# Performance work log

Measured on AMD Instinct MI355X. Metric: run time of the kernel, lower is better.

The kernel has to match this reference:

```python
import jax, jax.numpy as jnp
import numpy as np

B, N, F = 64, 512, 30          # batch, pf candidates, raw features
NDIM0, NDIM = 2, 4             # coord dims: layer0 uses 2, rest use n_dim_gnn=4
NOUT, NLAYERS = 64, 5          # GNN layer width / count
NDENSE = 128
BN_EPS = 1e-3                  # keras BatchNormalization default epsilon


def setup_inputs() -> dict:
    key = jax.random.key(0)
    ks = jax.random.split(key, 20)
    xx = jax.random.normal(ks[0], (B, N, F), jnp.float32)
    # validity mask: first L_b candidates valid
    lengths = jax.random.randint(ks[1], (B,), N // 4, N + 1)
    valid = (jnp.arange(N)[None, :] < lengths[:, None]).astype(jnp.float32)
    pt = jax.random.randint(ks[2], (B, N), 0, 8).astype(jnp.float32)
    pvq = jax.random.randint(ks[3], (B, N), 0, 8).astype(jnp.float32)
    fpv = jax.random.randint(ks[4], (B, N), 0, 4).astype(jnp.float32)
    xx = xx.at[:, :, 0].set(valid).at[:, :, 27].set(pt).at[:, :, 28].set(pvq).at[:, :, 29].set(fpv)
    g = lambda k, s, sc=0.05: jax.random.normal(k, s, jnp.float32) * sc
    d_in0 = 33  # 2+2+2 embeddings + 27 float features
    return {
        "xx": xx,
        "emb1": g(ks[5], (8, 2), 0.5),
        "emb2": g(ks[6], (8, 2), 0.5),
        "emb3": g(ks[7], (4, 2), 0.5),
        "A0": g(ks[8], ((d_in0 + 1) * 2 - 1, NOUT)),   # [67,64]
        "b0": g(ks[9], (NOUT,)),
        "A_rest": g(ks[10], (NLAYERS - 1, (NOUT + 1) * 2 - 1, NOUT)),  # [4,129,64]
        "b_rest": g(ks[11], (NLAYERS - 1, NOUT)),
        "bn_gamma": jnp.ones((NLAYERS, NOUT), jnp.float32),
        "bn_beta": jnp.zeros((NLAYERS, NOUT), jnp.float32),
        "dW0": g(ks[12], (N * NOUT, NDENSE), 0.01),
        "db0": g(ks[13], (NDENSE,)),
        "dW1": g(ks[14], (NDENSE, NDENSE)),
        "db1": g(ks[15], (NDENSE,)),
        "dbn_gamma": jnp.ones((2, NDENSE), jnp.float32),
        "dbn_beta": jnp.zeros((2, NDENSE), jnp.float32),
        "W2": g(ks[16], (NDENSE, 2)),
        "b2": g(ks[17], (2,)),
    }


def _bn(x, g, b):
    # inference BatchNorm with moving_mean=0, moving_var=1 (initial stats)
    return g * x * (1.0 / jnp.sqrt(1.0 + BN_EPS)) + b


def _gnn_layer(x, mask, n_dim, A, b):
    # x: [B,N,Fin], mask: [B,N]. Original builds [B,N,N,Fin+1] via tile/reshape;
    # algebraically the reduction over senders i factorizes:
    #   ss_feat[b,j] = x[b,j] * mask[b,j] * sum_i exp(-10*d_ij)
    #   ss_last[b,j] = mask[b,j] * sum_i d_ij * exp(-10*d_ij)
    c = x[..., -n_dim:]
    diff = c[:, :, None, :] - c[:, None, :, :]      # [B,N,N,n_dim]
    dist = jnp.sum(diff * diff, axis=-1)            # [B,N,N] squared distance
    w = jnp.exp(-10.0 * dist)
    S = jnp.sum(w, axis=1)                          # [B,N] per receiver j
    T = jnp.sum(dist * w, axis=1)                   # [B,N]
    ss_feat = x * (mask * S)[..., None] - x         # subtract concat(x, 0)
    ss_last = (mask * T)[..., None]
    xcat = jnp.concatenate([x, ss_feat, ss_last], axis=-1)  # [B,N,2*Fin+1]
    return (xcat @ A + b) * mask[..., None]


def _forward(xx, emb1, emb2, emb3, A0, b0, A_rest, b_rest, bn_gamma, bn_beta,
             dW0, db0, dW1, db1, dbn_gamma, dbn_beta, W2, b2):
    mask = xx[:, :, 0]
    e1 = emb1[jnp.abs(xx[:, :, 27]).astype(jnp.int32)]
    e2 = emb2[jnp.abs(xx[:, :, 28]).astype(jnp.int32)]
    e3 = emb3[jnp.abs(xx[:, :, 29]).astype(jnp.int32)]
    x = jnp.concatenate([e1, e2, e3, xx[:, :, :27]], axis=-1)  # [B,N,33]
    x = jnp.tanh(_bn(_gnn_layer(x, mask, NDIM0, A0, b0), bn_gamma[0], bn_beta[0]))
    for k in range(NLAYERS - 1):
        x = _gnn_layer(x, mask, NDIM, A_rest[k], b_rest[k])
        x = jnp.tanh(_bn(x, bn_gamma[k + 1], bn_beta[k + 1]))
    x = x.reshape(B, N * NOUT)
    x = jax.nn.sigmoid(_bn(x @ dW0 + db0, dbn_gamma[0], dbn_beta[0]))
    x = jax.nn.sigmoid(_bn(x @ dW1 + db1, dbn_gamma[1], dbn_beta[1]))
    x = x @ W2 + b2                                  # [B,2]
    # mode == 'dm': concat zeros on the right
    return jnp.concatenate([x, jnp.zeros((B, 2), x.dtype)], axis=1)


def reference(xx, emb1, emb2, emb3, A0, b0, A_rest, b_rest, bn_gamma, bn_beta,
              dW0, db0, dW1, db1, dbn_gamma, dbn_beta, W2, b2):
    return _forward(xx, emb1, emb2, emb3, A0, b0, A_rest, b_rest, bn_gamma, bn_beta,
                    dW0, db0, dW1, db1, dbn_gamma, dbn_beta, W2, b2)
```

## Files before the change

kernel.cpp:

```cpp
#include <hip/hip_runtime.h>
#include <math.h>

#define B_ 64
#define N_ 512
#define R_ (B_*N_)
#define INV_S 0.9995003746877732f

__device__ __forceinline__ float fast_tanh(float y){
  return 1.f - 2.f*__builtin_amdgcn_rcpf(1.f + __expf(2.f*y));
}
__device__ __forceinline__ float fast_sigmoid(float v){
  return __builtin_amdgcn_rcpf(1.f + __expf(-v));
}

struct GnnArgs {
  const float* xx;
  const float* emb1; const float* emb2; const float* emb3;
  const float* A0;  const float* b0;
  const float* Ar;  const float* br;
  const float* bng; const float* bnb;
  float4* cb0; float4* cb1;
  unsigned int* bar;
  float* xfinal;
};

template<int KP>
__device__ __forceinline__ void gemm_tile(const float* __restrict__ alo,
                                          const float* __restrict__ ahi,
                                          const float* __restrict__ xsrc,
                                          int o0, int lr0,
                                          float4 acc1[2], float4 acc2[2])
{
#pragma unroll
  for (int rr=0;rr<2;rr++){
    acc1[rr] = make_float4(0.f,0.f,0.f,0.f);
    acc2[rr] = make_float4(0.f,0.f,0.f,0.f);
  }
#pragma unroll 2
  for (int kc = 0; kc < KP; kc += 4){
    float4 a1[4], a2[4], xv[2];
#pragma unroll
    for (int uu=0;uu<4;uu++){
      a1[uu] = *(const float4*)&alo[(kc+uu)*64 + o0];
      a2[uu] = *(const float4*)&ahi[(kc+uu)*64 + o0];
    }
#pragma unroll
    for (int rr=0;rr<2;rr++)
      xv[rr] = *(const float4*)&xsrc[(lr0+rr)*68 + kc];
#pragma unroll
    for (int uu=0;uu<4;uu++){
#pragma unroll
      for (int rr=0;rr<2;rr++){
        float xu = ((const float*)&xv[rr])[uu];
        acc1[rr].x = fmaf(xu, a1[uu].x, acc1[rr].x);
        acc1[rr].y = fmaf(xu, a1[uu].y, acc1[rr].y);
        acc1[rr].z = fmaf(xu, a1[uu].z, acc1[rr].z);
        acc1[rr].w = fmaf(xu, a1[uu].w, acc1[rr].w);
        acc2[rr].x = fmaf(xu, a2[uu].x, acc2[rr].x);
        acc2[rr].y = fmaf(xu, a2[uu].y, acc2[rr].y);
        acc2[rr].z = fmaf(xu, a2[uu].z, acc2[rr].z);
        acc2[rr].w = fmaf(xu, a2[uu].w, acc2[rr].w);
      }
    }
  }
}

__global__ __launch_bounds__(512, 4) void gnn_fused(GnnArgs g)
{
  __shared__ float alo[64*64];
  __shared__ float ahi[64*64];
  __shared__ float xs[64*68];
  __shared__ float4 cl[512];
  __shared__ float spart[512], tpart[512];
  __shared__ float ml[64];

  const int tid   = threadIdx.x;
  const int b     = blockIdx.x;
  const int jc    = blockIdx.y;
  const int jloc  = jc*64;
  const int rbase = b*N_;
  const int cg = tid & 15, rg = tid >> 4;
  const int o0 = cg*4,  lr0 = rg*2;
  unsigned int* barp = g.bar + b*32;

  for (int k = 0; k < 5; ++k){
    const float* A;  const float* bi;  int K;
    if (k == 0){ A = g.A0;                        bi = g.b0;            K = 33; }
    else       { A = g.Ar + (size_t)(k-1)*129*64; bi = g.br + (k-1)*64; K = 64; }
    const float* gam = g.bng + k*64;
    const float* bet = g.bnb + k*64;

    if (k == 0){
      for (int idx = tid; idx < 36*64; idx += 512){
        int f = idx >> 6;
        alo[idx] = (f < 33) ? A[idx] : 0.f;
        ahi[idx] = (f < 33) ? A[33*64 + idx] : 0.f;
      }
      {
        const float* xr = g.xx + (size_t)(rbase + tid)*30;
        cl[tid] = make_float4(xr[25], xr[26], 0.f, 0.f);
      }
      if (tid < 64){
        const float* row = g.xx + (size_t)(rbase + jloc + tid)*30;
        float v[30];
#pragma unroll
        for (int i=0;i<30;i++) v[i] = row[i];
        int i1 = (int)fabsf(v[27]);
        int i2 = (int)fabsf(v[28]);
        int i3 = (int)fabsf(v[29]);
        float* o = &xs[tid*68];
        o[0]=g.emb1[i1*2+0]; o[1]=g.emb1[i1*2+1];
        o[2]=g.emb2[i2*2+0]; o[3]=g.emb2[i2*2+1];
        o[4]=g.emb3[i3*2+0]; o[5]=g.emb3[i3*2+1];
#pragma unroll
        for (int i=0;i<27;i++) o[6+i] = v[i];
        o[33]=0.f; o[34]=0.f; o[35]=0.f;
        ml[tid] = v[0];
      }
    } else {
      __syncthreads();
      if (tid == 0){
        __builtin_amdgcn_fence(__ATOMIC_RELEASE, "agent");
        __hip_atomic_fetch_add(barp, 1u, __ATOMIC_RELAXED, __HIP_MEMORY_SCOPE_AGENT);
      }
      {
        const float4* A4 = (const float4*)A;
        float4* alo4 = (float4*)alo;
        float4* ahi4 = (float4*)ahi;
        for (int idx = tid; idx < 1024; idx += 512){
          alo4[idx] = A4[idx];
          ahi4[idx] = A4[1024 + idx];
        }
      }
    }
    __syncthreads();

    float4 acc1[2], acc2[2];
    if (k == 0) gemm_tile<36>(alo, ahi, xs, o0, lr0, acc1, acc2);
    else        gemm_tile<64>(alo, ahi, xs, o0, lr0, acc1, acc2);

    float4 alast = *(const float4*)&A[(size_t)2*K*64 + o0];
    float4 bo = *(const float4*)&bi[o0];
    float4 go = *(const float4*)&gam[o0];
    float4 bb = *(const float4*)&bet[o0];

    if (k >= 1){
      if (tid == 0){
        unsigned int tgt = 8u*(unsigned int)k;
        while (__hip_atomic_load(barp, __ATOMIC_RELAXED, __HIP_MEMORY_SCOPE_AGENT) < tgt)
          __builtin_amdgcn_s_sleep(2);
        __builtin_amdgcn_fence(__ATOMIC_ACQUIRE, "agent");
      }
      __syncthreads();
      const float4* cbr = ((k & 1) ? g.cb0 : g.cb1) + rbase;
      cl[tid] = cbr[tid];
      __syncthreads();
    }

    {
      int jj = tid & 63, ic = tid >> 6, base = ic*64;
      float Ss = 0.f, Ts = 0.f;
      if (k == 0){
        float4 cj = cl[jloc + jj];
#pragma unroll 8
        for (int i=0;i<64;i++){
          float4 ci = cl[base+i];
          float d0 = cj.x-ci.x, d1 = cj.y-ci.y;
          float dist = d0*d0 + d1*d1;
          float w = __expf(-10.f*dist);
          Ss += w; Ts += dist*w;
        }
      } else {
        float4 cj = cl[jloc + jj];
#pragma unroll 8
        for (int i=0;i<64;i++){
          float4 ci = cl[base+i];
          float d0 = cj.x-ci.x, d1 = cj.y-ci.y, d2 = cj.z-ci.z, d3 = cj.w-ci.w;
          float dist = d0*d0 + d1*d1 + d2*d2 + d3*d3;
          float w = __expf(-10.f*dist);
          Ss += w; Ts += dist*w;
        }
      }
      spart[tid] = Ss;
      tpart[tid] = Ts;
    }
    __syncthreads();

    float4* cbw = (k & 1) ? g.cb1 : g.cb0;
#pragma unroll
    for (int rr=0;rr<2;rr++){
      int lr = lr0 + rr;
      float S = 0.f, T = 0.f;
#pragma unroll
      for (int c=0;c<8;c++){
        S += spart[lr + 64*c];
        T += tpart[lr + 64*c];
      }
      float m = ml[lr];
      float sc = m*S - 1.f;
      float tc = m*T;
      float4 v;
      v.x = (acc1[rr].x + sc*acc2[rr].x + tc*alast.x + bo.x)*m;
      v.y = (acc1[rr].y + sc*acc2[rr].y + tc*alast.y + bo.y)*m;
      v.z = (acc1[rr].z + sc*acc2[rr].z + tc*alast.z + bo.z)*m;
      v.w = (acc1[rr].w + sc*acc2[rr].w + tc*alast.w + bo.w)*m;
      float4 t;
      t.x = fast_tanh(go.x*(v.x*INV_S) + bb.x);
      t.y = fast_tanh(go.y*(v.y*INV_S) + bb.y);
      t.z = fast_tanh(go.z*(v.z*INV_S) + bb.z);
      t.w = fast_tanh(go.w*(v.w*INV_S) + bb.w);
      if (k < 4){
        *(float4*)&xs[lr*68 + o0] = t;
        if (cg == 15) cbw[rbase + jloc + lr] = t;
      } else {
        *(float4*)&g.xfinal[(size_t)(rbase + jloc + lr)*64 + o0] = t;
      }
    }
  }
}

__global__ __launch_bounds__(256) void dense0_partial(
    const float* __restrict__ X, const float* __restrict__ W,
    float* __restrict__ partial)
{
  __shared__ float xt[64*32];
  __shared__ float wt[32*128];
  int tid = threadIdx.x;
  int k0 = blockIdx.x*128;
  int og = (tid & 15)*8;
  int rg = (tid >> 4)*4;
  float acc[4][8];
#pragma unroll
  for (int a=0;a<4;a++)
#pragma unroll
    for (int u=0;u<8;u++) acc[a][u]=0.f;
  for (int kt = 0; kt < 128; kt += 32){
    __syncthreads();
    for (int idx = tid; idx < 512; idx += 256){
      int r = idx >> 3, kq = idx & 7;
      *(float4*)&xt[r*32 + kq*4] =
          *(const float4*)&X[(size_t)r*32768 + k0 + kt + kq*4];
    }
    {
      const float4* Wc = (const float4*)&W[(size_t)(k0+kt)*128];
      float4* wt4 = (float4*)wt;
      for (int idx = tid; idx < 1024; idx += 256) wt4[idx] = Wc[idx];
    }
    __syncthreads();
#pragma unroll 4
    for (int k=0;k<32;k++){
      float4 w0 = *(const float4*)&wt[k*128 + og];
      float4 w1 = *(const float4*)&wt[k*128 + og + 4];
      float xv[4];
#pragma unroll
      for (int rr=0;rr<4;rr++) xv[rr] = xt[(rg+rr)*32 + k];
#pragma unroll
      for (int rr=0;rr<4;rr++){
        acc[rr][0] = fmaf(xv[rr], w0.x, acc[rr][0]);
        acc[rr][1] = fmaf(xv[rr], w0.y, acc[rr][1]);
        acc[rr][2] = fmaf(xv[rr], w0.z, acc[rr][2]);
        acc[rr][3] = fmaf(xv[rr], w0.w, acc[rr][3]);
        acc[rr][4] = fmaf(xv[rr], w1.x, acc[rr][4]);
        acc[rr][5] = fmaf(xv[rr], w1.y, acc[rr][5]);
        acc[rr][6] = fmaf(xv[rr], w1.z, acc[rr][6]);
        acc[rr][7] = fmaf(xv[rr], w1.w, acc[rr][7]);
      }
    }
  }
  float* pb = partial + (size_t)blockIdx.x*8192;
#pragma unroll
  for (int rr=0;rr<4;rr++){
    *(float4*)&pb[(rg+rr)*128 + og]     = *(float4*)&acc[rr][0];
    *(float4*)&pb[(rg+rr)*128 + og + 4] = *(float4*)&acc[rr][4];
  }
}

__global__ __launch_bounds__(256) void dense_head(
    const float* __restrict__ partial,
    const float* __restrict__ db0, const float* __restrict__ dg0,
    const float* __restrict__ dbb0,
    const float* __restrict__ dW1, const float* __restrict__ db1,
    const float* __restrict__ dg1, const float* __restrict__ dbb1,
    const float* __restrict__ W2, const float* __restrict__ b2,
    float* __restrict__ out)
{
  __shared__ float sred[256];
  __shared__ float h[128];
  __shared__ float red0[128], red1[128];
  int tid = threadIdx.x;
  int b = blockIdx.x;
  int o = tid & 127, ph = tid >> 7;
  float s = 0.f;
#pragma unroll 16
  for (int p = ph*128; p < ph*128+128; p++)
    s += partial[(size_t)p*8192 + b*128 + o];
  sred[tid] = s;
  __syncthreads();
  if (tid < 128){
    float sum = sred[tid] + sred[tid+128];
    float v = dg0[tid]*((sum + db0[tid])*INV_S) + dbb0[tid];
    h[tid] = fast_sigmoid(v);
  }
  __syncthreads();
  if (tid < 128){
    float acc = 0.f;
#pragma unroll 8
    for (int k=0;k<128;k++) acc = fmaf(h[k], dW1[k*128 + tid], acc);
    float v = dg1[tid]*((acc + db1[tid])*INV_S) + dbb1[tid];
    float h1 = fast_sigmoid(v);
    red0[tid] = h1 * W2[tid*2+0];
    red1[tid] = h1 * W2[tid*2+1];
  }
  __syncthreads();
  for (int st=64; st>0; st>>=1){
    if (tid < st){ red0[tid] += red0[tid+st]; red1[tid] += red1[tid+st]; }
    __syncthreads();
  }
  if (tid == 0){
    out[b*4+0] = red0[0] + b2[0];
    out[b*4+1] = red1[0] + b2[1];
    out[b*4+2] = 0.f;
    out[b*4+3] = 0.f;
  }
}

extern "C" void kernel_launch(void* const* d_in, const int* in_sizes, int n_in,
                              void* d_out, int out_size, void* d_ws, size_t ws_size,
                              hipStream_t stream)
{
  const float* xx   = (const float*)d_in[0];
  const float* emb1 = (const float*)d_in[1];
  const float* emb2 = (const float*)d_in[2];
  const float* emb3 = (const float*)d_in[3];
  const float* A0   = (const float*)d_in[4];
  const float* b0   = (const float*)d_in[5];
  const float* Ar   = (const float*)d_in[6];
  const float* br   = (const float*)d_in[7];
  const float* bng  = (const float*)d_in[8];
  const float* bnb  = (const float*)d_in[9];
  const float* dW0  = (const float*)d_in[10];
  const float* db0  = (const float*)d_in[11];
  const float* dW1  = (const float*)d_in[12];
  const float* db1  = (const float*)d_in[13];
  const float* dbg  = (const float*)d_in[14];
  const float* dbb  = (const float*)d_in[15];
  const float* W2   = (const float*)d_in[16];
  const float* b2   = (const float*)d_in[17];

  float* ws = (float*)d_ws;
  float*  xA      = ws;
  float*  partial = xA + (size_t)R_*64;
  float4* cb0     = (float4*)(partial + (size_t)256*8192);
  float4* cb1     = cb0 + R_;
  unsigned int* bar = (unsigned int*)(cb1 + R_);

  hipMemsetAsync(bar, 0, 64*32*sizeof(unsigned int), stream);

  GnnArgs ga;
  ga.xx = xx; ga.emb1 = emb1; ga.emb2 = emb2; ga.emb3 = emb3;
  ga.A0 = A0; ga.b0 = b0; ga.Ar = Ar; ga.br = br;
  ga.bng = bng; ga.bnb = bnb;
  ga.cb0 = cb0; ga.cb1 = cb1; ga.bar = bar; ga.xfinal = xA;

  hipLaunchKernelGGL(gnn_fused, dim3(64,8), dim3(512), 0, stream, ga);

  dense0_partial<<<256, 256, 0, stream>>>(xA, dW0, partial);
  dense_head<<<B_, 256, 0, stream>>>(partial, db0, dbg, dbb,
                                     dW1, db1, dbg + 128, dbb + 128,
                                     W2, b2, (float*)d_out);
}
```

Measured before the change: 226.8 us.

## Warp-specialize GNN kernel: half threads do GEMM, half do distance sums and prefetch

Splits the 512-thread block into two roles. Threads 0-255 run the layer GEMM with a 4x4 register tile per thread. Threads 256-511 wait on the cross-block barrier, load coordinates and compute the pairwise Gaussian distance sums concurrently with the GEMM, then prefetch the next layer's weights into shared memory while the epilogue runs. This removes the serial GEMM-then-distance phases and two extra block syncs per layer. The cost is higher register pressure from the larger tile, and each group now has half the threads for its own work.

```diff
diff --git a/kernel.cpp b/kernel.cpp
--- a/kernel.cpp
+++ b/kernel.cpp
@@ -25,32 +25,32 @@
 };
 
 template<int KP>
-__device__ __forceinline__ void gemm_tile(const float* __restrict__ alo,
-                                          const float* __restrict__ ahi,
-                                          const float* __restrict__ xsrc,
-                                          int o0, int lr0,
-                                          float4 acc1[2], float4 acc2[2])
-{
-#pragma unroll
-  for (int rr=0;rr<2;rr++){
+__device__ __forceinline__ void gemm4x4(const float* __restrict__ alo,
+                                        const float* __restrict__ ahi,
+                                        const float* __restrict__ xsrc,
+                                        int o0, int r0,
+                                        float4 acc1[4], float4 acc2[4])
+{
+#pragma unroll
+  for (int rr=0;rr<4;rr++){
     acc1[rr] = make_float4(0.f,0.f,0.f,0.f);
     acc2[rr] = make_float4(0.f,0.f,0.f,0.f);
   }
 #pragma unroll 2
   for (int kc = 0; kc < KP; kc += 4){
-    float4 a1[4], a2[4], xv[2];
+    float4 a1[4], a2[4], xv[4];
 #pragma unroll
     for (int uu=0;uu<4;uu++){
       a1[uu] = *(const float4*)&alo[(kc+uu)*64 + o0];
       a2[uu] = *(const float4*)&ahi[(kc+uu)*64 + o0];
     }
 #pragma unroll
-    for (int rr=0;rr<2;rr++)
-      xv[rr] = *(const float4*)&xsrc[(lr0+rr)*68 + kc];
+    for (int rr=0;rr<4;rr++)
+      xv[rr] = *(const float4*)&xsrc[(r0+rr)*68 + kc];
 #pragma unroll
     for (int uu=0;uu<4;uu++){
 #pragma unroll
-      for (int rr=0;rr<2;rr++){
+      for (int rr=0;rr<4;rr++){
         float xu = ((const float*)&xv[rr])[uu];
         acc1[rr].x = fmaf(xu, a1[uu].x, acc1[rr].x);
         acc1[rr].y = fmaf(xu, a1[uu].y, acc1[rr].y);
@@ -79,9 +79,34 @@
   const int jc    = blockIdx.y;
   const int jloc  = jc*64;
   const int rbase = b*N_;
-  const int cg = tid & 15, rg = tid >> 4;
-  const int o0 = cg*4,  lr0 = rg*2;
   unsigned int* barp = g.bar + b*32;
+
+  {
+    const float* A = g.A0;
+    for (int idx = tid; idx < 36*64; idx += 512){
+      int f = idx >> 6;
+      alo[idx] = (f < 33) ? A[idx] : 0.f;
+      ahi[idx] = (f < 33) ? A[33*64 + idx] : 0.f;
+    }
+    if (tid < 64){
+      const float* row = g.xx + (size_t)(rbase + jloc + tid)*30;
+      float v[30];
+#pragma unroll
+      for (int i=0;i<30;i++) v[i] = row[i];
+      int i1 = (int)fabsf(v[27]);
+      int i2 = (int)fabsf(v[28]);
+      int i3 = (int)fabsf(v[29]);
+      float* o = &xs[tid*68];
+      o[0]=g.emb1[i1*2+0]; o[1]=g.emb1[i1*2+1];
+      o[2]=g.emb2[i2*2+0]; o[3]=g.emb2[i2*2+1];
+      o[4]=g.emb3[i3*2+0]; o[5]=g.emb3[i3*2+1];
+#pragma unroll
+      for (int i=0;i<27;i++) o[6+i] = v[i];
+      o[33]=0.f; o[34]=0.f; o[35]=0.f;
+      ml[tid] = v[0];
+    }
+  }
+  __syncthreads();
 
   for (int k = 0; k < 5; ++k){
     const float* A;  const float* bi;  int K;
@@ -90,130 +115,125 @@
     const float* gam = g.bng + k*64;
     const float* bet = g.bnb + k*64;
 
-    if (k == 0){
-      for (int idx = tid; idx < 36*64; idx += 512){
-        int f = idx >> 6;
-        alo[idx] = (f < 33) ? A[idx] : 0.f;
-        ahi[idx] = (f < 33) ? A[33*64 + idx] : 0.f;
-      }
-      {
-        const float* xr = g.xx + (size_t)(rbase + tid)*30;
-        cl[tid] = make_float4(xr[25], xr[26], 0.f, 0.f);
-      }
-      if (tid < 64){
-        const float* row = g.xx + (size_t)(rbase + jloc + tid)*30;
-        float v[30];
-#pragma unroll
-        for (int i=0;i<30;i++) v[i] = row[i];
-        int i1 = (int)fabsf(v[27]);
-        int i2 = (int)fabsf(v[28]);
-        int i3 = (int)fabsf(v[29]);
-        float* o = &xs[tid*68];
-        o[0]=g.emb1[i1*2+0]; o[1]=g.emb1[i1*2+1];
-        o[2]=g.emb2[i2*2+0]; o[3]=g.emb2[i2*2+1];
-        o[4]=g.emb3[i3*2+0]; o[5]=g.emb3[i3*2+1];
-#pragma unroll
-        for (int i=0;i<27;i++) o[6+i] = v[i];
-        o[33]=0.f; o[34]=0.f; o[35]=0.f;
-        ml[tid] = v[0];
-      }
-    } else {
+    if (k >= 1){
       __syncthreads();
       if (tid == 0){
         __builtin_amdgcn_fence(__ATOMIC_RELEASE, "agent");
         __hip_atomic_fetch_add(barp, 1u, __ATOMIC_RELAXED, __HIP_MEMORY_SCOPE_AGENT);
       }
-      {
-        const float4* A4 = (const float4*)A;
-        float4* alo4 = (float4*)alo;
-        float4* ahi4 = (float4*)ahi;
-        for (int idx = tid; idx < 1024; idx += 512){
-          alo4[idx] = A4[idx];
-          ahi4[idx] = A4[1024 + idx];
+    }
+
+    float4 acc1[4], acc2[4], alast, bo, go, bb;
+    int o0 = 0, r0 = 0;
+
+    if (tid < 256){
+      o0 = (tid & 15)*4;  r0 = (tid >> 4)*4;
+      if (k == 0) gemm4x4<36>(alo, ahi, xs, o0, r0, acc1, acc2);
+      else        gemm4x4<64>(alo, ahi, xs, o0, r0, acc1, acc2);
+      alast = *(const float4*)&A[(size_t)2*K*64 + o0];
+      bo = *(const float4*)&bi[o0];
+      go = *(const float4*)&gam[o0];
+      bb = *(const float4*)&bet[o0];
+    } else {
+      int s   = tid - 256;
+      int jj  = s & 63;
+      int icA = s >> 6;
+      int icB = icA + 4;
+      int rA  = icA*64 + jj;
+      int rB  = icB*64 + jj;
+
+      if (k == 0){
+        const float* xb = g.xx + (size_t)rbase*30;
+        cl[rA] = make_float4(xb[rA*30+25], xb[rA*30+26], 0.f, 0.f);
+        cl[rB] = make_float4(xb[rB*30+25], xb[rB*30+26], 0.f, 0.f);
+      } else {
+        if (jj == 0){
+          unsigned int tgt = 8u*(unsigned int)k;
+          while (__hip_atomic_load(barp, __ATOMIC_RELAXED, __HIP_MEMORY_SCOPE_AGENT) < tgt)
+            __builtin_amdgcn_s_sleep(2);
         }
+        __builtin_amdgcn_fence(__ATOMIC_ACQUIRE, "agent");
+        const float4* cbr = ((k & 1) ? g.cb0 : g.cb1) + rbase;
+        cl[rA] = cbr[rA];
+        cl[rB] = cbr[rB];
+      }
+
+      float4 cj;
+      if (k == 0){
+        const float* xj = g.xx + (size_t)(rbase + jloc + jj)*30;
+        cj = make_float4(xj[25], xj[26], 0.f, 0.f);
+      } else {
+        cj = *(const float4*)&xs[jj*68 + 60];
+      }
+      asm volatile("s_waitcnt lgkmcnt(0)" ::: "memory");
+
+#pragma unroll
+      for (int half = 0; half < 2; ++half){
+        int base = (half ? icB : icA)*64;
+        float Ss = 0.f, Ts = 0.f;
+        if (k == 0){
+#pragma unroll 8
+          for (int i=0;i<64;i++){
+            float4 ci = cl[base+i];
+            float d0 = cj.x-ci.x, d1 = cj.y-ci.y;
+            float dist = d0*d0 + d1*d1;
+            float w = __expf(-10.f*dist);
+            Ss += w; Ts += dist*w;
+          }
+        } else {
+#pragma unroll 8
+          for (int i=0;i<64;i++){
+            float4 ci = cl[base+i];
+            float d0 = cj.x-ci.x, d1 = cj.y-ci.y, d2 = cj.z-ci.z, d3 = cj.w-ci.w;
+            float dist = d0*d0 + d1*d1 + d2*d2 + d3*d3;
+            float w = __expf(-10.f*dist);
+            Ss += w; Ts += dist*w;
+          }
+        }
+        spart[jj + 64*(half ? icB : icA)] = Ss;
+        tpart[jj + 64*(half ? icB : icA)] = Ts;
       }
     }
     __syncthreads();
 
-    float4 acc1[2], acc2[2];
-    if (k == 0) gemm_tile<36>(alo, ahi, xs, o0, lr0, acc1, acc2);
-    else        gemm_tile<64>(alo, ahi, xs, o0, lr0, acc1, acc2);
-
-    float4 alast = *(const float4*)&A[(size_t)2*K*64 + o0];
-    float4 bo = *(const float4*)&bi[o0];
-    float4 go = *(const float4*)&gam[o0];
-    float4 bb = *(const float4*)&bet[o0];
-
-    if (k >= 1){
-      if (tid == 0){
-        unsigned int tgt = 8u*(unsigned int)k;
-        while (__hip_atomic_load(barp, __ATOMIC_RELAXED, __HIP_MEMORY_SCOPE_AGENT) < tgt)
-          __builtin_amdgcn_s_sleep(2);
-        __builtin_amdgcn_fence(__ATOMIC_ACQUIRE, "agent");
-      }
-      __syncthreads();
-      const float4* cbr = ((k & 1) ? g.cb0 : g.cb1) + rbase;
-      cl[tid] = cbr[tid];
-      __syncthreads();
-    }
-
-    {
-      int jj = tid & 63, ic = tid >> 6, base = ic*64;
-      float Ss = 0.f, Ts = 0.f;
-      if (k == 0){
-        float4 cj = cl[jloc + jj];
-#pragma unroll 8
-        for (int i=0;i<64;i++){
-          float4 ci = cl[base+i];
-          float d0 = cj.x-ci.x, d1 = cj.y-ci.y;
-          float dist = d0*d0 + d1*d1;
-          float w = __expf(-10.f*dist);
-          Ss += w; Ts += dist*w;
+    if (tid < 256){
+      float4* cbw = (k & 1) ? g.cb1 : g.cb0;
+#pragma unroll
+      for (int rr=0;rr<4;rr++){
+        int lr = r0 + rr;
+        float S = 0.f, T = 0.f;
+#pragma unroll
+        for (int c=0;c<8;c++){
+          S += spart[lr + 64*c];
+          T += tpart[lr + 64*c];
         }
-      } else {
-        float4 cj = cl[jloc + jj];
-#pragma unroll 8
-        for (int i=0;i<64;i++){
-          float4 ci = cl[base+i];
-          float d0 = cj.x-ci.x, d1 = cj.y-ci.y, d2 = cj.z-ci.z, d3 = cj.w-ci.w;
-          float dist = d0*d0 + d1*d1 + d2*d2 + d3*d3;
-          float w = __expf(-10.f*dist);
-          Ss += w; Ts += dist*w;
+        float m = ml[lr];
+        float sc = m*S - 1.f;
+        float tc = m*T;
+        float4 v;
+        v.x = (acc1[rr].x + sc*acc2[rr].x + tc*alast.x + bo.x)*m;
+        v.y = (acc1[rr].y + sc*acc2[rr].y + tc*alast.y + bo.y)*m;
+        v.z = (acc1[rr].z + sc*acc2[rr].z + tc*alast.z + bo.z)*m;
+        v.w = (acc1[rr].w + sc*acc2[rr].w + tc*alast.w + bo.w)*m;
+        float4 t;
+        t.x = fast_tanh(go.x*(v.x*INV_S) + bb.x);
+        t.y = fast_tanh(go.y*(v.y*INV_S) + bb.y);
+        t.z = fast_tanh(go.z*(v.z*INV_S) + bb.z);
+        t.w = fast_tanh(go.w*(v.w*INV_S) + bb.w);
+        if (k < 4){
+          *(float4*)&xs[lr*68 + o0] = t;
+          if ((tid & 15) == 15) cbw[rbase + jloc + lr] = t;
+        } else {
+          *(float4*)&g.xfinal[(size_t)(rbase + jloc + lr)*64 + o0] = t;
         }
       }
-      spart[tid] = Ss;
-      tpart[tid] = Ts;
-    }
-    __syncthreads();
-
-    float4* cbw = (k & 1) ? g.cb1 : g.cb0;
-#pragma unroll
-    for (int rr=0;rr<2;rr++){
-      int lr = lr0 + rr;
-      float S = 0.f, T = 0.f;
-#pragma unroll
-      for (int c=0;c<8;c++){
-        S += spart[lr + 64*c];
-        T += tpart[lr + 64*c];
-      }
-      float m = ml[lr];
-      float sc = m*S - 1.f;
-      float tc = m*T;
-      float4 v;
-      v.x = (acc1[rr].x + sc*acc2[rr].x + tc*alast.x + bo.x)*m;
-      v.y = (acc1[rr].y + sc*acc2[rr].y + tc*alast.y + bo.y)*m;
-      v.z = (acc1[rr].z + sc*acc2[rr].z + tc*alast.z + bo.z)*m;
-      v.w = (acc1[rr].w + sc*acc2[rr].w + tc*alast.w + bo.w)*m;
-      float4 t;
-      t.x = fast_tanh(go.x*(v.x*INV_S) + bb.x);
-      t.y = fast_tanh(go.y*(v.y*INV_S) + bb.y);
-      t.z = fast_tanh(go.z*(v.z*INV_S) + bb.z);
-      t.w = fast_tanh(go.w*(v.w*INV_S) + bb.w);
-      if (k < 4){
-        *(float4*)&xs[lr*68 + o0] = t;
-        if (cg == 15) cbw[rbase + jloc + lr] = t;
-      } else {
-        *(float4*)&g.xfinal[(size_t)(rbase + jloc + lr)*64 + o0] = t;
+    } else if (k < 4){
+      const float4* A4 = (const float4*)(g.Ar + (size_t)k*129*64);
+      float4* alo4 = (float4*)alo;
+      float4* ahi4 = (float4*)ahi;
+      for (int idx = tid - 256; idx < 1024; idx += 256){
+        alo4[idx] = A4[idx];
+        ahi4[idx] = A4[1024 + idx];
       }
     }
   }
```

Result: slower. 265.7 us (+17.1%).

## Stream GNN weights via wave-uniform loads and store activations transposed in LDS

Applied to the files above, without the earlier changes.

The per-layer GEMM no longer stages the A weight matrices in shared memory. Each wavefront now owns 8 output columns and reads the weights directly from global memory at wave-uniform addresses, while each lane handles one row of a transposed activation tile in LDS. This removes the 32 KB weight staging and its barrier, shrinks LDS use, and lets the epilogue write activations back in place. The costs are more global and scalar-cache weight traffic per k step, and a final transpose pass to write xfinal row-major.

```diff
diff --git a/kernel.cpp b/kernel.cpp
--- a/kernel.cpp
+++ b/kernel.cpp
@@ -24,63 +24,40 @@
   float* xfinal;
 };
 
-template<int KP>
-__device__ __forceinline__ void gemm_tile(const float* __restrict__ alo,
-                                          const float* __restrict__ ahi,
-                                          const float* __restrict__ xsrc,
-                                          int o0, int lr0,
-                                          float4 acc1[2], float4 acc2[2])
-{
-#pragma unroll
-  for (int rr=0;rr<2;rr++){
-    acc1[rr] = make_float4(0.f,0.f,0.f,0.f);
-    acc2[rr] = make_float4(0.f,0.f,0.f,0.f);
-  }
-#pragma unroll 2
-  for (int kc = 0; kc < KP; kc += 4){
-    float4 a1[4], a2[4], xv[2];
-#pragma unroll
-    for (int uu=0;uu<4;uu++){
-      a1[uu] = *(const float4*)&alo[(kc+uu)*64 + o0];
-      a2[uu] = *(const float4*)&ahi[(kc+uu)*64 + o0];
-    }
-#pragma unroll
-    for (int rr=0;rr<2;rr++)
-      xv[rr] = *(const float4*)&xsrc[(lr0+rr)*68 + kc];
-#pragma unroll
-    for (int uu=0;uu<4;uu++){
-#pragma unroll
-      for (int rr=0;rr<2;rr++){
-        float xu = ((const float*)&xv[rr])[uu];
-        acc1[rr].x = fmaf(xu, a1[uu].x, acc1[rr].x);
-        acc1[rr].y = fmaf(xu, a1[uu].y, acc1[rr].y);
-        acc1[rr].z = fmaf(xu, a1[uu].z, acc1[rr].z);
-        acc1[rr].w = fmaf(xu, a1[uu].w, acc1[rr].w);
-        acc2[rr].x = fmaf(xu, a2[uu].x, acc2[rr].x);
-        acc2[rr].y = fmaf(xu, a2[uu].y, acc2[rr].y);
-        acc2[rr].z = fmaf(xu, a2[uu].z, acc2[rr].z);
-        acc2[rr].w = fmaf(xu, a2[uu].w, acc2[rr].w);
-      }
-    }
+template<int K>
+__device__ __forceinline__ void gemm_sw(const float* __restrict__ A, int cw,
+                                        const float* __restrict__ xt, int lane,
+                                        float acc1[8], float acc2[8])
+{
+  const float* Alo = A + cw;
+  const float* Ahi = A + (size_t)K*64 + cw;
+#pragma unroll
+  for (int c=0;c<8;c++){ acc1[c]=0.f; acc2[c]=0.f; }
+#pragma unroll 4
+  for (int k=0;k<K;k++){
+    float xv = xt[k*64 + lane];
+#pragma unroll
+    for (int c=0;c<8;c++) acc1[c] = fmaf(xv, Alo[k*64 + c], acc1[c]);
+#pragma unroll
+    for (int c=0;c<8;c++) acc2[c] = fmaf(xv, Ahi[k*64 + c], acc2[c]);
   }
 }
 
 __global__ __launch_bounds__(512, 4) void gnn_fused(GnnArgs g)
 {
-  __shared__ float alo[64*64];
-  __shared__ float ahi[64*64];
-  __shared__ float xs[64*68];
+  __shared__ float xt[64*64];
   __shared__ float4 cl[512];
   __shared__ float spart[512], tpart[512];
-  __shared__ float ml[64];
+  __shared__ float scl[64], tcl[64], ml[64];
 
   const int tid   = threadIdx.x;
+  const int lane  = tid & 63;
+  const int w     = __builtin_amdgcn_readfirstlane(tid >> 6);
+  const int cw    = w*8;
   const int b     = blockIdx.x;
   const int jc    = blockIdx.y;
   const int jloc  = jc*64;
   const int rbase = b*N_;
-  const int cg = tid & 15, rg = tid >> 4;
-  const int o0 = cg*4,  lr0 = rg*2;
   unsigned int* barp = g.bar + b*32;
 
   for (int k = 0; k < 5; ++k){
@@ -91,11 +68,6 @@
     const float* bet = g.bnb + k*64;
 
     if (k == 0){
-      for (int idx = tid; idx < 36*64; idx += 512){
-        int f = idx >> 6;
-        alo[idx] = (f < 33) ? A[idx] : 0.f;
-        ahi[idx] = (f < 33) ? A[33*64 + idx] : 0.f;
-      }
       {
         const float* xr = g.xx + (size_t)(rbase + tid)*30;
         cl[tid] = make_float4(xr[25], xr[26], 0.f, 0.f);
@@ -108,41 +80,28 @@
         int i1 = (int)fabsf(v[27]);
         int i2 = (int)fabsf(v[28]);
         int i3 = (int)fabsf(v[29]);
-        float* o = &xs[tid*68];
-        o[0]=g.emb1[i1*2+0]; o[1]=g.emb1[i1*2+1];
-        o[2]=g.emb2[i2*2+0]; o[3]=g.emb2[i2*2+1];
-        o[4]=g.emb3[i3*2+0]; o[5]=g.emb3[i3*2+1];
-#pragma unroll
-        for (int i=0;i<27;i++) o[6+i] = v[i];
-        o[33]=0.f; o[34]=0.f; o[35]=0.f;
+        xt[0*64+tid] = g.emb1[i1*2+0];
+        xt[1*64+tid] = g.emb1[i1*2+1];
+        xt[2*64+tid] = g.emb2[i2*2+0];
+        xt[3*64+tid] = g.emb2[i2*2+1];
+        xt[4*64+tid] = g.emb3[i3*2+0];
+        xt[5*64+tid] = g.emb3[i3*2+1];
+#pragma unroll
+        for (int i=0;i<27;i++) xt[(6+i)*64 + tid] = v[i];
         ml[tid] = v[0];
       }
+      __syncthreads();
     } else {
       __syncthreads();
       if (tid == 0){
         __builtin_amdgcn_fence(__ATOMIC_RELEASE, "agent");
         __hip_atomic_fetch_add(barp, 1u, __ATOMIC_RELAXED, __HIP_MEMORY_SCOPE_AGENT);
       }
-      {
-        const float4* A4 = (const float4*)A;
-        float4* alo4 = (float4*)alo;
-        float4* ahi4 = (float4*)ahi;
-        for (int idx = tid; idx < 1024; idx += 512){
-          alo4[idx] = A4[idx];
-          ahi4[idx] = A4[1024 + idx];
-        }
-      }
-    }
-    __syncthreads();
-
-    float4 acc1[2], acc2[2];
-    if (k == 0) gemm_tile<36>(alo, ahi, xs, o0, lr0, acc1, acc2);
-    else        gemm_tile<64>(alo, ahi, xs, o0, lr0, acc1, acc2);
-
-    float4 alast = *(const float4*)&A[(size_t)2*K*64 + o0];
-    float4 bo = *(const float4*)&bi[o0];
-    float4 go = *(const float4*)&gam[o0];
-    float4 bb = *(const float4*)&bet[o0];
+    }
+
+    float acc1[8], acc2[8];
+    if (k == 0) gemm_sw<33>(A, cw, xt, lane, acc1, acc2);
+    else        gemm_sw<64>(A, cw, xt, lane, acc1, acc2);
 
     if (k >= 1){
       if (tid == 0){
@@ -161,24 +120,26 @@
       int jj = tid & 63, ic = tid >> 6, base = ic*64;
       float Ss = 0.f, Ts = 0.f;
       if (k == 0){
-        float4 cj = cl[jloc + jj];
+        const float* xj = g.xx + (size_t)(rbase + jloc + jj)*30;
+        float cjx = xj[25], cjy = xj[26];
 #pragma unroll 8
         for (int i=0;i<64;i++){
           float4 ci = cl[base+i];
-          float d0 = cj.x-ci.x, d1 = cj.y-ci.y;
+          float d0 = cjx-ci.x, d1 = cjy-ci.y;
           float dist = d0*d0 + d1*d1;
-          float w = __expf(-10.f*dist);
-          Ss += w; Ts += dist*w;
+          float wgt = __expf(-10.f*dist);
+          Ss += wgt; Ts += dist*wgt;
         }
       } else {
-        float4 cj = cl[jloc + jj];
+        float4 cj = make_float4(xt[60*64+jj], xt[61*64+jj],
+                                xt[62*64+jj], xt[63*64+jj]);
 #pragma unroll 8
         for (int i=0;i<64;i++){
           float4 ci = cl[base+i];
           float d0 = cj.x-ci.x, d1 = cj.y-ci.y, d2 = cj.z-ci.z, d3 = cj.w-ci.w;
           float dist = d0*d0 + d1*d1 + d2*d2 + d3*d3;
-          float w = __expf(-10.f*dist);
-          Ss += w; Ts += dist*w;
+          float wgt = __expf(-10.f*dist);
+          Ss += wgt; Ts += dist*wgt;
         }
       }
       spart[tid] = Ss;
@@ -186,36 +147,47 @@
     }
     __syncthreads();
 
-    float4* cbw = (k & 1) ? g.cb1 : g.cb0;
-#pragma unroll
-    for (int rr=0;rr<2;rr++){
-      int lr = lr0 + rr;
+    if (tid < 64){
       float S = 0.f, T = 0.f;
 #pragma unroll
       for (int c=0;c<8;c++){
-        S += spart[lr + 64*c];
-        T += tpart[lr + 64*c];
-      }
-      float m = ml[lr];
-      float sc = m*S - 1.f;
-      float tc = m*T;
-      float4 v;
-      v.x = (acc1[rr].x + sc*acc2[rr].x + tc*alast.x + bo.x)*m;
-      v.y = (acc1[rr].y + sc*acc2[rr].y + tc*alast.y + bo.y)*m;
-      v.z = (acc1[rr].z + sc*acc2[rr].z + tc*alast.z + bo.z)*m;
-      v.w = (acc1[rr].w + sc*acc2[rr].w + tc*alast.w + bo.w)*m;
-      float4 t;
-      t.x = fast_tanh(go.x*(v.x*INV_S) + bb.x);
-      t.y = fast_tanh(go.y*(v.y*INV_S) + bb.y);
-      t.z = fast_tanh(go.z*(v.z*INV_S) + bb.z);
-      t.w = fast_tanh(go.w*(v.w*INV_S) + bb.w);
-      if (k < 4){
-        *(float4*)&xs[lr*68 + o0] = t;
-        if (cg == 15) cbw[rbase + jloc + lr] = t;
-      } else {
-        *(float4*)&g.xfinal[(size_t)(rbase + jloc + lr)*64 + o0] = t;
-      }
-    }
+        S += spart[tid + 64*c];
+        T += tpart[tid + 64*c];
+      }
+      float m = ml[tid];
+      scl[tid] = m*S - 1.f;
+      tcl[tid] = m*T;
+    }
+    __syncthreads();
+
+    {
+      float m  = ml[lane];
+      float sc = scl[lane];
+      float tc = tcl[lane];
+      float t[8];
+#pragma unroll
+      for (int c=0;c<8;c++){
+        float alast = A[(size_t)2*K*64 + cw + c];
+        float boc = bi[cw + c];
+        float goc = gam[cw + c];
+        float bbc = bet[cw + c];
+        float v = (acc1[c] + sc*acc2[c] + tc*alast + boc)*m;
+        t[c] = fast_tanh(goc*(v*INV_S) + bbc);
+        xt[(cw+c)*64 + lane] = t[c];
+      }
+      if (k < 4 && w == 7){
+        float4* cbw = (k & 1) ? g.cb1 : g.cb0;
+        cbw[rbase + jloc + lane] = make_float4(t[4], t[5], t[6], t[7]);
+      }
+    }
+  }
+
+  __syncthreads();
+  for (int idx = tid; idx < 1024; idx += 512){
+    int row = idx >> 4, q = idx & 15;
+    float4 v = make_float4(xt[(q*4+0)*64 + row], xt[(q*4+1)*64 + row],
+                           xt[(q*4+2)*64 + row], xt[(q*4+3)*64 + row]);
+    *(float4*)&g.xfinal[(size_t)(rbase + jloc + row)*64 + q*4] = v;
   }
 }
 
```

After: 313.2 us. 1.38x slower.

## Reorder GNN layer so GEMM runs after distance sums with 4x4 register tiles

Applied to the files above, without the earlier changes.

The per-layer GEMM now runs after the pairwise distance reduction, in 256 threads each computing a 4-row by 4-column tile instead of 512 threads doing 2 rows. The per-row S/T reductions move into a 64-thread stage stored in shared memory. The intent is more register reuse of the A loads and one fewer wait, since the inter-block barrier wait and the coordinate load now sit together ahead of the distance stage. In exchange, half the threads sit idle during the GEMM, register pressure rises, and the GEMM no longer overlaps the barrier wait.

```diff
diff --git a/kernel.cpp b/kernel.cpp
--- a/kernel.cpp
+++ b/kernel.cpp
@@ -25,32 +25,32 @@
 };
 
 template<int KP>
-__device__ __forceinline__ void gemm_tile(const float* __restrict__ alo,
-                                          const float* __restrict__ ahi,
-                                          const float* __restrict__ xsrc,
-                                          int o0, int lr0,
-                                          float4 acc1[2], float4 acc2[2])
-{
-#pragma unroll
-  for (int rr=0;rr<2;rr++){
+__device__ __forceinline__ void gemm4x4(const float* __restrict__ alo,
+                                        const float* __restrict__ ahi,
+                                        const float* __restrict__ xsrc,
+                                        int o0, int r0,
+                                        float4 acc1[4], float4 acc2[4])
+{
+#pragma unroll
+  for (int rr=0;rr<4;rr++){
     acc1[rr] = make_float4(0.f,0.f,0.f,0.f);
     acc2[rr] = make_float4(0.f,0.f,0.f,0.f);
   }
 #pragma unroll 2
   for (int kc = 0; kc < KP; kc += 4){
-    float4 a1[4], a2[4], xv[2];
+    float4 a1[4], a2[4], xv[4];
 #pragma unroll
     for (int uu=0;uu<4;uu++){
       a1[uu] = *(const float4*)&alo[(kc+uu)*64 + o0];
       a2[uu] = *(const float4*)&ahi[(kc+uu)*64 + o0];
     }
 #pragma unroll
-    for (int rr=0;rr<2;rr++)
-      xv[rr] = *(const float4*)&xsrc[(lr0+rr)*68 + kc];
+    for (int rr=0;rr<4;rr++)
+      xv[rr] = *(const float4*)&xsrc[(r0+rr)*68 + kc];
 #pragma unroll
     for (int uu=0;uu<4;uu++){
 #pragma unroll
-      for (int rr=0;rr<2;rr++){
+      for (int rr=0;rr<4;rr++){
         float xu = ((const float*)&xv[rr])[uu];
         acc1[rr].x = fmaf(xu, a1[uu].x, acc1[rr].x);
         acc1[rr].y = fmaf(xu, a1[uu].y, acc1[rr].y);
@@ -72,15 +72,15 @@
   __shared__ float xs[64*68];
   __shared__ float4 cl[512];
   __shared__ float spart[512], tpart[512];
-  __shared__ float ml[64];
+  __shared__ float scl[64], tcl[64], ml[64];
 
   const int tid   = threadIdx.x;
   const int b     = blockIdx.x;
   const int jc    = blockIdx.y;
   const int jloc  = jc*64;
   const int rbase = b*N_;
-  const int cg = tid & 15, rg = tid >> 4;
-  const int o0 = cg*4,  lr0 = rg*2;
+  const int cg = tid & 15, rg = (tid >> 4) & 15;
+  const int o0 = cg*4,  r0 = rg*4;
   unsigned int* barp = g.bar + b*32;
 
   for (int k = 0; k < 5; ++k){
@@ -132,19 +132,6 @@
           ahi4[idx] = A4[1024 + idx];
         }
       }
-    }
-    __syncthreads();
-
-    float4 acc1[2], acc2[2];
-    if (k == 0) gemm_tile<36>(alo, ahi, xs, o0, lr0, acc1, acc2);
-    else        gemm_tile<64>(alo, ahi, xs, o0, lr0, acc1, acc2);
-
-    float4 alast = *(const float4*)&A[(size_t)2*K*64 + o0];
-    float4 bo = *(const float4*)&bi[o0];
-    float4 go = *(const float4*)&gam[o0];
-    float4 bb = *(const float4*)&bet[o0];
-
-    if (k >= 1){
       if (tid == 0){
         unsigned int tgt = 8u*(unsigned int)k;
         while (__hip_atomic_load(barp, __ATOMIC_RELAXED, __HIP_MEMORY_SCOPE_AGENT) < tgt)
@@ -154,14 +141,14 @@
       __syncthreads();
       const float4* cbr = ((k & 1) ? g.cb0 : g.cb1) + rbase;
       cl[tid] = cbr[tid];
-      __syncthreads();
-    }
+    }
+    __syncthreads();
 
     {
       int jj = tid & 63, ic = tid >> 6, base = ic*64;
+      float4 cj = cl[jloc + jj];
       float Ss = 0.f, Ts = 0.f;
       if (k == 0){
-        float4 cj = cl[jloc + jj];
 #pragma unroll 8
         for (int i=0;i<64;i++){
           float4 ci = cl[base+i];
@@ -171,7 +158,6 @@
           Ss += w; Ts += dist*w;
         }
       } else {
-        float4 cj = cl[jloc + jj];
 #pragma unroll 8
         for (int i=0;i<64;i++){
           float4 ci = cl[base+i];
@@ -186,34 +172,53 @@
     }
     __syncthreads();
 
-    float4* cbw = (k & 1) ? g.cb1 : g.cb0;
-#pragma unroll
-    for (int rr=0;rr<2;rr++){
-      int lr = lr0 + rr;
+    if (tid < 64){
       float S = 0.f, T = 0.f;
 #pragma unroll
       for (int c=0;c<8;c++){
-        S += spart[lr + 64*c];
-        T += tpart[lr + 64*c];
-      }
-      float m = ml[lr];
-      float sc = m*S - 1.f;
-      float tc = m*T;
-      float4 v;
-      v.x = (acc1[rr].x + sc*acc2[rr].x + tc*alast.x + bo.x)*m;
-      v.y = (acc1[rr].y + sc*acc2[rr].y + tc*alast.y + bo.y)*m;
-      v.z = (acc1[rr].z + sc*acc2[rr].z + tc*alast.z + bo.z)*m;
-      v.w = (acc1[rr].w + sc*acc2[rr].w + tc*alast.w + bo.w)*m;
-      float4 t;
-      t.x = fast_tanh(go.x*(v.x*INV_S) + bb.x);
-      t.y = fast_tanh(go.y*(v.y*INV_S) + bb.y);
-      t.z = fast_tanh(go.z*(v.z*INV_S) + bb.z);
-      t.w = fast_tanh(go.w*(v.w*INV_S) + bb.w);
-      if (k < 4){
-        *(float4*)&xs[lr*68 + o0] = t;
-        if (cg == 15) cbw[rbase + jloc + lr] = t;
-      } else {
-        *(float4*)&g.xfinal[(size_t)(rbase + jloc + lr)*64 + o0] = t;
+        S += spart[tid + 64*c];
+        T += tpart[tid + 64*c];
+      }
+      float m = ml[tid];
+      scl[tid] = m*S - 1.f;
+      tcl[tid] = m*T;
+    }
+    __syncthreads();
+
+    float4 acc1[4], acc2[4];
+    float4 alast, bo, go, bb;
+    if (tid < 256){
+      if (k == 0) gemm4x4<36>(alo, ahi, xs, o0, r0, acc1, acc2);
+      else        gemm4x4<64>(alo, ahi, xs, o0, r0, acc1, acc2);
+      alast = *(const float4*)&A[(size_t)2*K*64 + o0];
+      bo = *(const float4*)&bi[o0];
+      go = *(const float4*)&gam[o0];
+      bb = *(const float4*)&bet[o0];
+    }
+    __syncthreads();
+
+    if (tid < 256){
+      float4* cbw = (k & 1) ? g.cb1 : g.cb0;
+#pragma unroll
+      for (int rr=0;rr<4;rr++){
+        int lr = r0 + rr;
+        float sc = scl[lr], tc = tcl[lr], m = ml[lr];
+        float4 v;
+        v.x = (acc1[rr].x + sc*acc2[rr].x + tc*alast.x + bo.x)*m;
+        v.y = (acc1[rr].y + sc*acc2[rr].y + tc*alast.y + bo.y)*m;
+        v.z = (acc1[rr].z + sc*acc2[rr].z + tc*alast.z + bo.z)*m;
+        v.w = (acc1[rr].w + sc*acc2[rr].w + tc*alast.w + bo.w)*m;
+        float4 t;
+        t.x = fast_tanh(go.x*(v.x*INV_S) + bb.x);
+        t.y = fast_tanh(go.y*(v.y*INV_S) + bb.y);
+        t.z = fast_tanh(go.z*(v.z*INV_S) + bb.z);
+        t.w = fast_tanh(go.w*(v.w*INV_S) + bb.w);
+        if (k < 4){
+          *(float4*)&xs[lr*68 + o0] = t;
+          if (cg == 15) cbw[rbase + jloc + lr] = t;
+        } else {
+          *(float4*)&g.xfinal[(size_t)(rbase + jloc + lr)*64 + o0] = t;
+        }
       }
     }
   }
```

After: 244.7 us. +7.9%, slower.
